# Kernel tuning notes

Measured on AMD Instinct MI355X. Metric: run time of the kernel, lower is better.

The kernel has to match this reference:

```python
import jax, jax.numpy as jnp
import numpy as np
import math

N = 2048          # rows (forced: input_dim_B // 2)
DB = 4096         # input_dim_B
DA = 5120         # input_dim_A
DX2 = DA - DB     # 1024, X2 feature dim
M1, M2 = 8, 4
DK, DV1, DV2 = 64, 64, 64
M = 512           # d_model of trailing encoder layers (nhead=1 inside)
LN_EPS = 1e-5


def setup_inputs() -> dict:
    key = jax.random.key(0)
    ks = jax.random.split(key, 24)
    s = 0.02
    f32 = jnp.float32
    inp = {
        "X1": jax.random.normal(ks[0], (N, DB), f32),
        "X2": jax.random.normal(ks[1], (N, DX2), f32),
        "X3": jax.random.normal(ks[2], (N, DB), f32),
        # Type-A heads (stacked over m1)
        "WQ": jax.random.normal(ks[3], (M1, DA, DK), f32) * s,
        "WK": jax.random.normal(ks[4], (M1, DA, DK), f32) * s,
        "WV": jax.random.normal(ks[5], (M1, DA, DV1), f32) * s,
        # Type-B heads (stacked over m2)
        "WVB": jax.random.normal(ks[6], (M2, DX2, DV2), f32) * s,
        "W_ali": jax.random.normal(ks[7], (DB, DB // 2), f32) * s,
        "W_O": jax.random.normal(ks[8], (M1 * DV1 + M2 * DV2, M), f32) * s,
        # two TransformerEncoderLayers (post-LN, nhead=1, relu FFN), stacked over layer dim
        "enc_Wq": jax.random.normal(ks[9], (2, M, M), f32) * s,
        "enc_Wk": jax.random.normal(ks[10], (2, M, M), f32) * s,
        "enc_Wv": jax.random.normal(ks[11], (2, M, M), f32) * s,
        "enc_bq": jnp.zeros((2, M), f32),
        "enc_bk": jnp.zeros((2, M), f32),
        "enc_bv": jnp.zeros((2, M), f32),
        "enc_Wo": jax.random.normal(ks[12], (2, M, M), f32) * s,
        "enc_bo": jnp.zeros((2, M), f32),
        "enc_ln1_g": jnp.ones((2, M), f32),
        "enc_ln1_b": jnp.zeros((2, M), f32),
        "enc_W1": jax.random.normal(ks[13], (2, M, DV1), f32) * s,
        "enc_b1": jnp.zeros((2, DV1), f32),
        "enc_W2": jax.random.normal(ks[14], (2, DV1, M), f32) * s,
        "enc_b2": jnp.zeros((2, M), f32),
        "enc_ln2_g": jnp.ones((2, M), f32),
        "enc_ln2_b": jnp.zeros((2, M), f32),
    }
    return inp


def _layer_norm(x, g, b):
    mu = jnp.mean(x, axis=-1, keepdims=True)
    var = jnp.mean(jnp.square(x - mu), axis=-1, keepdims=True)
    return (x - mu) * jax.lax.rsqrt(var + LN_EPS) * g + b


def _encoder_layer(x, Wq, bq, Wk, bk, Wv, bv, Wo, bo, g1, b1, W1, bW1, W2, bW2, g2, b2):
    # post-norm TransformerEncoderLayer, nhead=1, dropout in eval mode (off)
    q = x @ Wq + bq
    k = x @ Wk + bk
    v = x @ Wv + bv
    att = jax.nn.softmax((q @ k.T) / math.sqrt(M), axis=-1) @ v
    x = _layer_norm(x + (att @ Wo + bo), g1, b1)
    f = jax.nn.relu(x @ W1 + bW1) @ W2 + bW2
    return _layer_norm(x + f, g2, b2)


def reference(X1, X2, X3, WQ, WK, WV, WVB, W_ali, W_O,
              enc_Wq, enc_bq, enc_Wk, enc_bk, enc_Wv, enc_bv, enc_Wo, enc_bo,
              enc_ln1_g, enc_ln1_b, enc_W1, enc_b1, enc_W2, enc_b2, enc_ln2_g, enc_ln2_b):
    XA = jnp.concatenate([X1, X2], axis=1)  # [N, DA]
    # Type-A heads, batched over m1
    Q = jnp.einsum('nd,hdk->hnk', XA, WQ)
    K = jnp.einsum('nd,hdk->hnk', XA, WK)
    V = jnp.einsum('nd,hdv->hnv', XA, WV)
    scores = jnp.einsum('hnk,hmk->hnm', Q, K) / math.sqrt(DK)
    S = jax.nn.softmax(scores, axis=1)  # torch softmax(dim=0): over query/row axis
    ZA = jnp.einsum('hnm,hmv->hnv', S, V)             # [m1, N, dv1]
    ZA = jnp.transpose(ZA, (1, 0, 2)).reshape(N, M1 * DV1)
    # Type-B heads
    ali = jax.nn.sigmoid(X3) @ W_ali                  # [N, N] (DB//2 == N)
    zb = jnp.einsum('nd,hdv->hnv', X2, WVB)           # [m2, N, dv2]
    ZB = jnp.einsum('nm,hmv->hnv', ali, zb)
    ZB = jnp.transpose(ZB, (1, 0, 2)).reshape(N, M2 * DV2)
    Z = jnp.concatenate([ZA, ZB], axis=1) @ W_O       # [N, M]
    for l in range(2):
        Z = _encoder_layer(Z, enc_Wq[l], enc_bq[l], enc_Wk[l], enc_bk[l],
                           enc_Wv[l], enc_bv[l], enc_Wo[l], enc_bo[l],
                           enc_ln1_g[l], enc_ln1_b[l], enc_W1[l], enc_b1[l],
                           enc_W2[l], enc_b2[l], enc_ln2_g[l], enc_ln2_b[l])
    return Z
```

## Files before the change

kernel.cpp:

```cpp
#include <hip/hip_runtime.h>

#define DEV __device__ __forceinline__

typedef __attribute__((ext_vector_type(4))) float f32x4;
typedef __attribute__((ext_vector_type(8))) short s16x8;

DEV ushort f2b(float f) {
  union { float f; unsigned u; } x; x.f = f;
  unsigned r = (x.u + 0x7FFFu + ((x.u >> 16) & 1u)) >> 16;
  return (ushort)r;
}
DEV float b2f(ushort u) {
  union { unsigned u; float f; } x; x.u = ((unsigned)u) << 16;
  return x.f;
}

DEV void gload16(const ushort* g, ushort* l) {
  __builtin_amdgcn_global_load_lds(
      (const __attribute__((address_space(1))) unsigned int*)g,
      (__attribute__((address_space(3))) unsigned int*)l, 16, 0, 0);
}

struct PtrList { const float* p[4]; };

template<int BM, int BN, int BIAS, int ACT, bool OF, bool OB, int SKX,
         bool CSTAT, bool RSTAT, int NBUF>
__global__ __launch_bounds__(256) void gemm(
    const ushort* __restrict__ A, int lda, long long sA,
    const ushort* __restrict__ B, int ldb, long long sB,
    float* __restrict__ Cf, ushort* __restrict__ Cb, int ldc, long long sC,
    const float* __restrict__ bias, const float* __restrict__ bias2,
    float* __restrict__ pmo, float* __restrict__ pso,
    float scale0, float scale1, int K)
{
  constexpr int WM = BM / 2, WN = BN / 2, FM = WM / 16, FN = WN / 16;
  __shared__ __align__(16) ushort As[NBUF][BM * 64];
  __shared__ __align__(16) ushort Bs[NBUF][BN * 64];
  const int tid = threadIdx.x, l = tid & 63, w = tid >> 6;
  const int wr = w >> 1, wc = w & 1;
  const int gx = gridDim.x, gy = gridDim.y;
  const int nwg = gx * gy;
  const int orig = blockIdx.y * gx + blockIdx.x;
  const int xcd = orig & 7, rest = orig >> 3;
  const int q8 = nwg >> 3, r8 = nwg & 7;
  const int f = (xcd < r8 ? xcd * (q8 + 1) : r8 * (q8 + 1) + (xcd - r8) * q8) + rest;
  int bxr = f / gy;
  const int byy = f - bxr * gy;
  int ks = 0;
  if constexpr (SKX > 1) {
    const int nbx = gx / SKX;
    ks = bxr / nbx; bxr -= ks * nbx;
  }
  const int brow = byy * BM, bcol = bxr * BN;
  const long long z = blockIdx.z;
  A += z * sA + (size_t)ks * K;
  B += z * sB + (size_t)ks * K;
  const int lr = l & 15;
  const int sw = lr & 7, kh = l >> 4;
  f32x4 acc[FM][FN] = {};
  const int nk = K >> 6;

  auto stage = [&](int kt, int buf) {
    const int kof = kt << 6;
#pragma unroll
    for (int i = 0; i < BM / 32; ++i) {
      const int c = i * 256 + tid;
      const int r = c >> 3, k8 = c & 7;
      gload16(A + (size_t)(brow + r) * lda + kof + ((k8 ^ (r & 7)) << 3),
              &As[buf][i * 2048 + w * 512]);
    }
#pragma unroll
    for (int i = 0; i < BN / 32; ++i) {
      const int c = i * 256 + tid;
      const int r = c >> 3, k8 = c & 7;
      gload16(B + (size_t)(bcol + r) * ldb + kof + ((k8 ^ (r & 7)) << 3),
              &Bs[buf][i * 2048 + w * 512]);
    }
  };

  auto compute = [&](int kt, int buf) {
#pragma unroll
    for (int kk = 0; kk < 2; ++kk) {
      const int koff = ((kk * 4 + kh) ^ sw) << 3;
      s16x8 af[FM], bf[FN];
#pragma unroll
      for (int m = 0; m < FM; ++m)
        af[m] = *(const s16x8*)&As[buf][(wr * WM + m * 16 + lr) * 64 + koff];
#pragma unroll
      for (int n = 0; n < FN; ++n)
        bf[n] = *(const s16x8*)&Bs[buf][(wc * WN + n * 16 + lr) * 64 + koff];
#pragma unroll
      for (int m = 0; m < FM; ++m)
#pragma unroll
        for (int n = 0; n < FN; ++n)
          acc[m][n] = __builtin_amdgcn_mfma_f32_16x16x32_bf16(af[m], bf[n], acc[m][n], 0, 0, 0);
    }
  };

  if constexpr (NBUF == 2) {
    stage(0, 0);
    __syncthreads();
    for (int kt = 0; kt < nk - 1; ++kt) {
      stage(kt + 1, (kt + 1) & 1);
      compute(kt, kt & 1);
      __syncthreads();
    }
    compute(nk - 1, (nk - 1) & 1);
  } else {
    for (int kt = 0; kt < nk; ++kt) {
      stage(kt, 0);
      __syncthreads();
      compute(kt, 0);
      __syncthreads();
    }
  }

  if constexpr (OF || OB) {
    const float sc = (z == 0) ? scale0 : scale1;
    const float* bp = (z == 0) ? bias : bias2;
    const int cr = (l >> 4) * 4, cc = l & 15;
#pragma unroll
    for (int m = 0; m < FM; ++m) {
      const int r0 = brow + wr * WM + m * 16 + cr;
#pragma unroll
      for (int n = 0; n < FN; ++n) {
        const int gc = bcol + wc * WN + n * 16 + cc;
        float bc = 0.f;
        if constexpr (BIAS == 1) bc = bp[gc];
#pragma unroll
        for (int j = 0; j < 4; ++j) {
          float v = acc[m][n][j];
          if constexpr (BIAS == 1) v += bc;
          if constexpr (BIAS == 2) v += bp[r0 + j];
          v *= sc;
          if constexpr (ACT == 1) v = fmaxf(v, 0.f);
          const size_t off = (size_t)(r0 + j) * ldc + gc + (size_t)((z * SKX + ks) * sC);
          if constexpr (OF) Cf[off] = v;
          if constexpr (OB) Cb[off] = f2b(v);
        }
      }
    }
  }

  if constexpr (CSTAT) {
    __shared__ float sM[2][2][FN][16], sS[2][2][FN][16];
    float mx[FN], se[FN];
#pragma unroll
    for (int n = 0; n < FN; ++n) {
      float m0 = -3e38f;
#pragma unroll
      for (int m = 0; m < FM; ++m)
#pragma unroll
        for (int j = 0; j < 4; ++j) m0 = fmaxf(m0, acc[m][n][j]);
      float s0 = 0.f;
#pragma unroll
      for (int m = 0; m < FM; ++m)
#pragma unroll
        for (int j = 0; j < 4; ++j) s0 += __expf(acc[m][n][j] - m0);
      mx[n] = m0; se[n] = s0;
    }
#pragma unroll
    for (int o = 16; o <= 32; o <<= 1) {
#pragma unroll
      for (int n = 0; n < FN; ++n) {
        float m2 = __shfl_xor(mx[n], o), s2 = __shfl_xor(se[n], o);
        float M = fmaxf(mx[n], m2);
        se[n] = se[n] * __expf(mx[n] - M) + s2 * __expf(m2 - M);
        mx[n] = M;
      }
    }
    __syncthreads();
    if (l < 16) {
#pragma unroll
      for (int n = 0; n < FN; ++n) { sM[wr][wc][n][l] = mx[n]; sS[wr][wc][n][l] = se[n]; }
    }
    __syncthreads();
    if (wr == 0 && l < 16) {
#pragma unroll
      for (int n = 0; n < FN; ++n) {
        float m1 = sM[0][wc][n][l], m2 = sM[1][wc][n][l];
        float s1 = sS[0][wc][n][l], s2 = sS[1][wc][n][l];
        float M = fmaxf(m1, m2);
        float S = s1 * __expf(m1 - M) + s2 * __expf(m2 - M);
        const int gc = bcol + wc * 32 + n * 16 + l;
        const size_t o = ((size_t)(z * gy + byy)) * 2048 + gc;
        pmo[o] = M; pso[o] = S;
      }
    }
  }

  if constexpr (RSTAT) {
    __shared__ float sRM[2][2][WM], sRS[2][2][WM];
#pragma unroll
    for (int m = 0; m < FM; ++m) {
#pragma unroll
      for (int j = 0; j < 4; ++j) {
        float m0 = -3e38f;
#pragma unroll
        for (int n = 0; n < FN; ++n) m0 = fmaxf(m0, acc[m][n][j]);
        float s0 = 0.f;
#pragma unroll
        for (int n = 0; n < FN; ++n) s0 += __expf(acc[m][n][j] - m0);
#pragma unroll
        for (int o = 1; o <= 8; o <<= 1) {
          float m2 = __shfl_xor(m0, o), s2 = __shfl_xor(s0, o);
          float M = fmaxf(m0, m2);
          s0 = s0 * __expf(m0 - M) + s2 * __expf(m2 - M);
          m0 = M;
        }
        if ((l & 15) == 0) {
          sRM[wr][wc][m * 16 + (l >> 4) * 4 + j] = m0;
          sRS[wr][wc][m * 16 + (l >> 4) * 4 + j] = s0;
        }
      }
    }
    __syncthreads();
    if (wc == 0) {
      float m1 = sRM[wr][0][l], m2 = sRM[wr][1][l];
      float s1 = sRS[wr][0][l], s2 = sRS[wr][1][l];
      float M = fmaxf(m1, m2);
      float S = s1 * __expf(m1 - M) + s2 * __expf(m2 - M);
      const size_t o = (size_t)bxr * 2048 + brow + wr * WM + l;
      pmo[o] = M; pso[o] = S;
    }
  }
}

template<int MH, int NH>
DEV void qmfma2(const s16x8 (&Ax)[8], const s16x8 (&Bf)[4], f32x4 (&acc)[8][4]) {
#pragma unroll
  for (int kk = 0; kk < 2; ++kk)
#pragma unroll
    for (int m = 0; m < 4; ++m)
#pragma unroll
      for (int n = 0; n < 2; ++n)
        acc[MH * 4 + m][NH * 2 + n] = __builtin_amdgcn_mfma_f32_16x16x32_bf16(
            Ax[kk * 4 + m], Bf[kk * 2 + n], acc[MH * 4 + m][NH * 2 + n], 0, 0, 0);
}

DEV void tailwait(int c) {
  if (c == 1) { asm volatile("s_waitcnt vmcnt(4)" ::: "memory"); }
  else if (c == 2) { asm volatile("s_waitcnt vmcnt(0)" ::: "memory"); }
}

#define GBAR() asm volatile("s_barrier" ::: "memory")

template<int NBX>
__global__ __launch_bounds__(512, 2) void gemm256(
    const ushort* __restrict__ A, int lda,
    const ushort* __restrict__ B, int ldb,
    ushort* __restrict__ Cb, int ldc, long long sC, int Kc)
{
  __shared__ __align__(16) ushort As[2][2][8192];
  __shared__ __align__(16) ushort Bs[2][2][8192];
  const int tid = threadIdx.x, l = tid & 63, w = tid >> 6;
  const int wr = w >> 2, wc = w & 3;
  const int gx = gridDim.x, gy = gridDim.y;
  const int nwg = gx * gy;
  const int orig = blockIdx.y * gx + blockIdx.x;
  const int xcd = orig & 7, rest = orig >> 3;
  const int q8 = nwg >> 3, r8 = nwg & 7;
  const int f = (xcd < r8 ? xcd * (q8 + 1) : r8 * (q8 + 1) + (xcd - r8) * q8) + rest;
  int bxr = f / gy;
  const int byy = f - bxr * gy;
  const int ks = bxr / NBX; bxr -= ks * NBX;
  const int brow = byy * 256, bcol = bxr * 256;
  A += (size_t)ks * Kc;
  B += (size_t)ks * Kc;
  const int nk = Kc >> 6;
  const int lr = l & 15, kh = l >> 4, sw = lr & 7;
  const int arow = wr * 64 + lr, brw = wc * 32 + lr;

  const int r0 = tid >> 3, k80 = tid & 7;
  const size_t aoff = (size_t)(brow + r0) * lda + ((k80 ^ (r0 & 7)) << 3);
  const size_t boff = (size_t)(bcol + r0) * ldb + ((k80 ^ (r0 & 7)) << 3);

  f32x4 acc[8][4] = {};
  s16x8 Ax[8];
  s16x8 B0s[4], B1s[4];

  auto stA = [&](int kt, int buf, int half) {
    if (kt >= nk) return;
    const ushort* s = A + aoff + (size_t)(half * 128) * lda + (kt << 6);
    gload16(s, &As[buf][half][w * 512]);
    gload16(s + (size_t)64 * lda, &As[buf][half][4096 + w * 512]);
  };
  auto stB = [&](int kt, int buf, int half) {
    if (kt >= nk) return;
    const ushort* s = B + boff + (size_t)(half * 128) * ldb + (kt << 6);
    gload16(s, &Bs[buf][half][w * 512]);
    gload16(s + (size_t)64 * ldb, &Bs[buf][half][4096 + w * 512]);
  };
  auto rdA = [&](int buf, int half) {
#pragma unroll
    for (int kk = 0; kk < 2; ++kk) {
      const int koff = ((kk * 4 + kh) ^ sw) << 3;
#pragma unroll
      for (int m = 0; m < 4; ++m)
        Ax[kk * 4 + m] = *(const s16x8*)&As[buf][half][(arow + m * 16) * 64 + koff];
    }
  };
  auto rdB = [&](s16x8 (&dst)[4], int buf, int half) {
#pragma unroll
    for (int kk = 0; kk < 2; ++kk) {
      const int koff = ((kk * 4 + kh) ^ sw) << 3;
#pragma unroll
      for (int n = 0; n < 2; ++n)
        dst[kk * 2 + n] = *(const s16x8*)&Bs[buf][half][(brw + n * 16) * 64 + koff];
    }
  };

  stA(0, 0, 0); stB(0, 0, 0); stA(0, 0, 1); stB(0, 0, 1);
  stA(1, 1, 0); stB(1, 1, 0);
  asm volatile("s_waitcnt vmcnt(4)" ::: "memory");
  GBAR();
  rdA(0, 0); rdB(B0s, 0, 0);

  const int NT2 = nk >> 1;
#pragma unroll 1
  for (int j = 0; j < NT2; ++j) {
    const int tb = 2 * j + 1, ta2 = 2 * j + 2, tb2 = 2 * j + 3;
    const bool more = (ta2 < nk);
    stA(tb, 1, 1); GBAR();
    rdB(B1s, 0, 1);
    __builtin_amdgcn_s_setprio(1); qmfma2<0, 0>(Ax, B0s, acc); __builtin_amdgcn_s_setprio(0);
    GBAR();
    stB(tb, 1, 1); GBAR();
    __builtin_amdgcn_s_setprio(1); qmfma2<0, 1>(Ax, B1s, acc); __builtin_amdgcn_s_setprio(0);
    GBAR();
    stA(ta2, 0, 0); GBAR();
    rdA(0, 1);
    __builtin_amdgcn_s_setprio(1); qmfma2<1, 0>(Ax, B0s, acc); __builtin_amdgcn_s_setprio(0);
    GBAR();
    stB(ta2, 0, 0); GBAR();
    __builtin_amdgcn_s_setprio(1); qmfma2<1, 1>(Ax, B1s, acc); __builtin_amdgcn_s_setprio(0);
    tailwait(more ? 1 : 2); GBAR();
    rdA(1, 0); rdB(B0s, 1, 0);
    stA(ta2, 0, 1); GBAR();
    rdB(B1s, 1, 1);
    __builtin_amdgcn_s_setprio(1); qmfma2<0, 0>(Ax, B0s, acc); __builtin_amdgcn_s_setprio(0);
    GBAR();
    stB(ta2, 0, 1); GBAR();
    __builtin_amdgcn_s_setprio(1); qmfma2<0, 1>(Ax, B1s, acc); __builtin_amdgcn_s_setprio(0);
    GBAR();
    stA(tb2, 1, 0); GBAR();
    rdA(1, 1);
    __builtin_amdgcn_s_setprio(1); qmfma2<1, 0>(Ax, B0s, acc); __builtin_amdgcn_s_setprio(0);
    GBAR();
    stB(tb2, 1, 0); GBAR();
    __builtin_amdgcn_s_setprio(1); qmfma2<1, 1>(Ax, B1s, acc); __builtin_amdgcn_s_setprio(0);
    tailwait(more ? 1 : 0); GBAR();
    if (more) { rdA(0, 0); rdB(B0s, 0, 0); }
  }

  ushort* out = Cb + (size_t)ks * sC;
  const int cr = kh * 4, cc = lr;
#pragma unroll
  for (int mh = 0; mh < 2; ++mh)
#pragma unroll
    for (int m = 0; m < 4; ++m) {
      const int ro = brow + mh * 128 + wr * 64 + m * 16 + cr;
#pragma unroll
      for (int nh = 0; nh < 2; ++nh)
#pragma unroll
        for (int n = 0; n < 2; ++n) {
          const int gc = bcol + nh * 128 + wc * 32 + n * 16 + cc;
#pragma unroll
          for (int j2 = 0; j2 < 4; ++j2)
            out[(size_t)(ro + j2) * ldc + gc] = f2b(acc[mh * 4 + m][nh * 2 + n][j2]);
        }
    }
}

__global__ __launch_bounds__(256) void ffn_fused(
    const ushort* __restrict__ X, const ushort* __restrict__ W1,
    const float* __restrict__ b1, const ushort* __restrict__ W2T,
    const float* __restrict__ b2, float* __restrict__ Y)
{
  __shared__ __align__(16) ushort As[64 * 64];
  __shared__ __align__(16) ushort Bs[64 * 64];
  __shared__ __align__(16) ushort Hs[64 * 64];
  const int tid = threadIdx.x, l = tid & 63, w = tid >> 6;
  const int wr = w >> 1, wc = w & 1;
  const int bx = blockIdx.x, brow = blockIdx.y * 64;
  const int lr = l & 15, g = l >> 4, sw = lr & 7;
  f32x4 acc[2][2] = {};
  for (int kt = 0; kt < 8; ++kt) {
    const int kof = kt << 6;
#pragma unroll
    for (int i = 0; i < 2; ++i) {
      const int c = i * 256 + tid, r = c >> 3, k8 = c & 7;
      gload16(X + (size_t)(brow + r) * 512 + kof + ((k8 ^ (r & 7)) << 3),
              &As[i * 2048 + w * 512]);
    }
#pragma unroll
    for (int i = 0; i < 2; ++i) {
      const int c = i * 256 + tid, r = c >> 3, k8 = c & 7;
      gload16(W1 + (size_t)r * 512 + kof + ((k8 ^ (r & 7)) << 3),
              &Bs[i * 2048 + w * 512]);
    }
    __syncthreads();
#pragma unroll
    for (int kk = 0; kk < 2; ++kk) {
      const int koff = ((kk * 4 + g) ^ sw) << 3;
      s16x8 af[2], bf[2];
#pragma unroll
      for (int m = 0; m < 2; ++m) af[m] = *(const s16x8*)&As[(wr * 32 + m * 16 + lr) * 64 + koff];
#pragma unroll
      for (int n = 0; n < 2; ++n) bf[n] = *(const s16x8*)&Bs[(wc * 32 + n * 16 + lr) * 64 + koff];
#pragma unroll
      for (int m = 0; m < 2; ++m)
#pragma unroll
        for (int n = 0; n < 2; ++n)
          acc[m][n] = __builtin_amdgcn_mfma_f32_16x16x32_bf16(af[m], bf[n], acc[m][n], 0, 0, 0);
    }
    __syncthreads();
  }
#pragma unroll
  for (int m = 0; m < 2; ++m)
#pragma unroll
    for (int n = 0; n < 2; ++n) {
      const int col = wc * 32 + n * 16 + lr;
      const float bb = b1[col];
#pragma unroll
      for (int j = 0; j < 4; ++j) {
        const int row = wr * 32 + m * 16 + g * 4 + j;
        Hs[row * 64 + (((col >> 3) ^ (row & 7)) << 3) + (col & 7)] =
            f2b(fmaxf(acc[m][n][j] + bb, 0.f));
      }
    }
#pragma unroll
  for (int i = 0; i < 2; ++i) {
    const int c = i * 256 + tid, r = c >> 3, k8 = c & 7;
    gload16(W2T + (size_t)(bx * 64 + r) * 64 + ((k8 ^ (r & 7)) << 3),
            &Bs[i * 2048 + w * 512]);
  }
  __syncthreads();
  f32x4 acc2[2][2] = {};
#pragma unroll
  for (int kk = 0; kk < 2; ++kk) {
    const int koff = ((kk * 4 + g) ^ sw) << 3;
    s16x8 af[2], bf[2];
#pragma unroll
    for (int m = 0; m < 2; ++m) af[m] = *(const s16x8*)&Hs[(wr * 32 + m * 16 + lr) * 64 + koff];
#pragma unroll
    for (int n = 0; n < 2; ++n) bf[n] = *(const s16x8*)&Bs[(wc * 32 + n * 16 + lr) * 64 + koff];
#pragma unroll
    for (int m = 0; m < 2; ++m)
#pragma unroll
      for (int n = 0; n < 2; ++n)
        acc2[m][n] = __builtin_amdgcn_mfma_f32_16x16x32_bf16(af[m], bf[n], acc2[m][n], 0, 0, 0);
  }
#pragma unroll
  for (int m = 0; m < 2; ++m)
#pragma unroll
    for (int n = 0; n < 2; ++n) {
      const int gc = bx * 64 + wc * 32 + n * 16 + lr;
      const float bb = b2[gc];
#pragma unroll
      for (int j = 0; j < 4; ++j) {
        const int row = brow + wr * 32 + m * 16 + g * 4 + j;
        Y[(size_t)row * 512 + gc] = acc2[m][n][j] + bb;
      }
    }
}

__global__ __launch_bounds__(256) void pv_fused(
    const ushort* __restrict__ Q, const ushort* __restrict__ K,
    const ushort* __restrict__ Vt, const float* __restrict__ lse,
    ushort* __restrict__ ZAP)
{
  __shared__ __align__(16) ushort Qs[64 * 64];
  __shared__ __align__(16) ushort Ks[2][64 * 64];
  __shared__ __align__(16) ushort Vs[2][64 * 64];
  __shared__ __align__(16) ushort Ps[64 * 64];
  __shared__ float Ls[512];
  const int tid = threadIdx.x, l = tid & 63, w = tid >> 6;
  const int wr = w >> 1, wc = w & 1;
  const int h = blockIdx.z, brow = blockIdx.x * 64, ms = blockIdx.y;
  const int lr = l & 15, g = l >> 4, sw = lr & 7;

  auto stageKV = [&](int mc, int buf) {
#pragma unroll
    for (int i = 0; i < 2; ++i) {
      const int c = i * 256 + tid, r = c >> 3, k8 = c & 7;
      gload16(K + (size_t)(mc * 64 + r) * 512 + h * 64 + ((k8 ^ (r & 7)) << 3),
              &Ks[buf][i * 2048 + w * 512]);
    }
#pragma unroll
    for (int i = 0; i < 2; ++i) {
      const int c = i * 256 + tid, r = c >> 3, k8 = c & 7;
      gload16(Vt + (size_t)(h * 64 + r) * 2048 + mc * 64 + ((k8 ^ (r & 7)) << 3),
              &Vs[buf][i * 2048 + w * 512]);
    }
  };

#pragma unroll
  for (int i = 0; i < 2; ++i) {
    const int c = i * 256 + tid, r = c >> 3, k8 = c & 7;
    gload16(Q + (size_t)(brow + r) * 512 + h * 64 + ((k8 ^ (r & 7)) << 3),
            &Qs[i * 2048 + w * 512]);
  }
  stageKV(ms * 8, 0);
  for (int i = tid; i < 512; i += 256) Ls[i] = lse[h * 2048 + ms * 512 + i];
  __syncthreads();

  s16x8 aq[2][2];
#pragma unroll
  for (int nf = 0; nf < 2; ++nf)
#pragma unroll
    for (int kk = 0; kk < 2; ++kk)
      aq[nf][kk] = *(const s16x8*)&Qs[(wr * 32 + nf * 16 + lr) * 64 + (((kk * 4 + g) ^ sw) << 3)];

  f32x4 zacc[2][2] = {};
  for (int mi = 0; mi < 8; ++mi) {
    const int mc = ms * 8 + mi;
    const int buf = mi & 1;
    if (mi < 7) stageKV(mc + 1, buf ^ 1);
    f32x4 sacc[2][2] = {};
#pragma unroll
    for (int kk = 0; kk < 2; ++kk) {
      const int koff = ((kk * 4 + g) ^ sw) << 3;
      s16x8 bk[2];
#pragma unroll
      for (int mf = 0; mf < 2; ++mf)
        bk[mf] = *(const s16x8*)&Ks[buf][(wc * 32 + mf * 16 + lr) * 64 + koff];
#pragma unroll
      for (int nf = 0; nf < 2; ++nf)
#pragma unroll
        for (int mf = 0; mf < 2; ++mf)
          sacc[nf][mf] = __builtin_amdgcn_mfma_f32_16x16x32_bf16(aq[nf][kk], bk[mf], sacc[nf][mf], 0, 0, 0);
    }
#pragma unroll
    for (int nf = 0; nf < 2; ++nf)
#pragma unroll
      for (int mf = 0; mf < 2; ++mf) {
        const int m_loc = wc * 32 + mf * 16 + lr;
        const float lv = Ls[mi * 64 + m_loc];
#pragma unroll
        for (int j = 0; j < 4; ++j) {
          const int n_loc = wr * 32 + nf * 16 + g * 4 + j;
          Ps[n_loc * 64 + (((m_loc >> 3) ^ (n_loc & 7)) << 3) + (m_loc & 7)] =
              f2b(__expf(sacc[nf][mf][j] - lv));
        }
      }
    __syncthreads();
#pragma unroll
    for (int kk = 0; kk < 2; ++kk) {
      const int koff = ((kk * 4 + g) ^ sw) << 3;
      s16x8 pa[2], bv[2];
#pragma unroll
      for (int nf = 0; nf < 2; ++nf)
        pa[nf] = *(const s16x8*)&Ps[(wr * 32 + nf * 16 + lr) * 64 + koff];
#pragma unroll
      for (int vf = 0; vf < 2; ++vf)
        bv[vf] = *(const s16x8*)&Vs[buf][(wc * 32 + vf * 16 + lr) * 64 + koff];
#pragma unroll
      for (int nf = 0; nf < 2; ++nf)
#pragma unroll
        for (int vf = 0; vf < 2; ++vf)
          zacc[nf][vf] = __builtin_amdgcn_mfma_f32_16x16x32_bf16(pa[nf], bv[vf], zacc[nf][vf], 0, 0, 0);
    }
    __syncthreads();
  }
  ushort* out = ZAP + (size_t)ms * 2048 * 512;
#pragma unroll
  for (int nf = 0; nf < 2; ++nf)
#pragma unroll
    for (int vf = 0; vf < 2; ++vf)
#pragma unroll
      for (int j = 0; j < 4; ++j) {
        const int n = brow + wr * 32 + nf * 16 + g * 4 + j;
        const int col = h * 64 + wc * 32 + vf * 16 + lr;
        out[(size_t)n * 512 + col] = f2b(zacc[nf][vf][j]);
      }
}

template<int NS, int ACT>
__global__ __launch_bounds__(256) void reduceN(const ushort* __restrict__ P, long long sC,
    ushort* __restrict__ out, int cols, int ldout, long long zPoff, long long zOoff,
    int cshift, long long bstride, float scale, int scThresh, int rows,
    const float* __restrict__ bias)
{
  P += blockIdx.z * zPoff; out += blockIdx.z * zOoff;
  const int c4n = cols >> 2;
  const size_t total = (size_t)rows * c4n;
  for (size_t i = (size_t)blockIdx.x * 256 + threadIdx.x; i < total; i += (size_t)gridDim.x * 256) {
    const size_t r = i / c4n;
    const int c4 = (int)(i - r * c4n) << 2;
    float4 s = make_float4(0.f, 0.f, 0.f, 0.f);
#pragma unroll
    for (int k = 0; k < NS; ++k) {
      ushort4 t = *(const ushort4*)(P + (size_t)k * sC + r * cols + c4);
      s.x += b2f(t.x); s.y += b2f(t.y); s.z += b2f(t.z); s.w += b2f(t.w);
    }
    if constexpr (ACT == 1) {
      float4 bb = *(const float4*)(bias + c4);
      s.x = fmaxf(s.x + bb.x, 0.f); s.y = fmaxf(s.y + bb.y, 0.f);
      s.z = fmaxf(s.z + bb.z, 0.f); s.w = fmaxf(s.w + bb.w, 0.f);
    }
    const float sc = (c4 < scThresh) ? scale : 1.f;
    ushort4 o;
    o.x = f2b(s.x * sc); o.y = f2b(s.y * sc); o.z = f2b(s.z * sc); o.w = f2b(s.w * sc);
    const size_t oo = r * ldout + (size_t)(c4 >> cshift) * bstride + (c4 & ((1 << cshift) - 1));
    *(ushort4*)(out + oo) = o;
  }
}

__global__ __launch_bounds__(256) void prep_xab(const float* __restrict__ X1,
    const float* __restrict__ X2, ushort* __restrict__ XAb) {
  const size_t total = (size_t)2048 * 1280;
  for (size_t i = (size_t)blockIdx.x * 256 + threadIdx.x; i < total; i += (size_t)gridDim.x * 256) {
    const size_t r = i / 1280;
    const int c = (int)(i - r * 1280) << 2;
    float4 v = (c < 4096) ? *(const float4*)(X1 + r * 4096 + c)
                          : *(const float4*)(X2 + r * 1024 + (c - 4096));
    ushort4 o; o.x = f2b(v.x); o.y = f2b(v.y); o.z = f2b(v.z); o.w = f2b(v.w);
    *(ushort4*)(XAb + r * 5120 + c) = o;
  }
}

__global__ __launch_bounds__(256) void prep_x3w(const float* __restrict__ X3,
    const float* __restrict__ Wali, ushort* __restrict__ sX3,
    ushort* __restrict__ Walib) {
  const size_t n1 = (size_t)2048 * 1024;
  const size_t n2 = (size_t)4096 * 512;
  const size_t total = n1 + n2;
  for (size_t i = (size_t)blockIdx.x * 256 + threadIdx.x; i < total; i += (size_t)gridDim.x * 256) {
    if (i < n1) {
      const size_t r = i / 1024;
      const int c = (int)(i - r * 1024) << 2;
      float4 v = *(const float4*)(X3 + r * 4096 + c);
      v.x = 1.f / (1.f + __expf(-v.x)); v.y = 1.f / (1.f + __expf(-v.y));
      v.z = 1.f / (1.f + __expf(-v.z)); v.w = 1.f / (1.f + __expf(-v.w));
      ushort4 o; o.x = f2b(v.x); o.y = f2b(v.y); o.z = f2b(v.z); o.w = f2b(v.w);
      *(ushort4*)(sX3 + r * 4096 + c) = o;
    } else {
      const size_t j = i - n1;
      const size_t r = j / 512;
      const int c = (int)(j - r * 512) << 2;
      float4 v = *(const float4*)(Wali + r * 2048 + c);
      ushort4 o; o.x = f2b(v.x); o.y = f2b(v.y); o.z = f2b(v.z); o.w = f2b(v.w);
      *(ushort4*)(Walib + r * 2048 + c) = o;
    }
  }
}

__global__ __launch_bounds__(256) void expconv_row(const float* __restrict__ S,
    const float* __restrict__ pm, const float* __restrict__ ps, ushort* __restrict__ P) {
  const int r = blockIdx.x;
  float m = pm[(size_t)(threadIdx.x & 31) * 2048 + r];
  float s = ps[(size_t)(threadIdx.x & 31) * 2048 + r];
#pragma unroll
  for (int o = 1; o < 32; o <<= 1) {
    float m2 = __shfl_xor(m, o), s2 = __shfl_xor(s, o);
    float M = fmaxf(m, m2);
    s = s * __expf(m - M) + s2 * __expf(m2 - M);
    m = M;
  }
  const float L = m + __logf(s);
  const float* row = S + (size_t)r * 2048;
  ushort* pr = P + (size_t)r * 2048;
  for (int c = threadIdx.x * 4; c < 2048; c += 1024) {
    float4 v = *(const float4*)(row + c);
    ushort4 o4;
    o4.x = f2b(__expf(v.x - L)); o4.y = f2b(__expf(v.y - L));
    o4.z = f2b(__expf(v.z - L)); o4.w = f2b(__expf(v.w - L));
    *(ushort4*)(pr + c) = o4;
  }
}

__global__ __launch_bounds__(256) void colcombine(const float* __restrict__ pm,
    const float* __restrict__ ps, float* __restrict__ lse) {
  const int id = blockIdx.x * 256 + threadIdx.x;
  const int h = id >> 11, c = id & 2047;
  float M = -3e38f;
#pragma unroll
  for (int s = 0; s < 16; ++s) M = fmaxf(M, pm[((size_t)(h * 16 + s)) * 2048 + c]);
  float S = 0.f;
#pragma unroll
  for (int s = 0; s < 16; ++s) {
    size_t o = ((size_t)(h * 16 + s)) * 2048 + c;
    S += ps[o] * __expf(pm[o] - M);
  }
  lse[id] = M + __logf(S);
}

__global__ __launch_bounds__(256) void transpose_conv_multi(PtrList in, int zPerT,
    ushort* __restrict__ out, int R, int C) {
  __shared__ ushort t[32][33];
  const int z = blockIdx.z;
  const float* ip = in.p[z / zPerT] + (size_t)(z % zPerT) * R * C;
  ushort* op = out + (size_t)z * R * C;
  const int r0 = blockIdx.x * 32, c0 = blockIdx.y * 32;
#pragma unroll
  for (int i = 0; i < 4; ++i) {
    int r = r0 + threadIdx.y + i * 8;
    int c = c0 + threadIdx.x;
    float v = (r < R && c < C) ? ip[(size_t)r * C + c] : 0.f;
    t[threadIdx.x][threadIdx.y + i * 8] = f2b(v);
  }
  __syncthreads();
#pragma unroll
  for (int i = 0; i < 4; ++i) {
    int c = c0 + threadIdx.y + i * 8;
    int r = r0 + threadIdx.x;
    if (c < C && r < R) op[(size_t)c * R + r] = t[threadIdx.y + i * 8][threadIdx.x];
  }
}

__global__ __launch_bounds__(256) void transpose_conv_batch(
    const float* __restrict__ WVB, ushort* __restrict__ WVBT,
    const float* __restrict__ W_O, ushort* __restrict__ WOT,
    const float* __restrict__ eW1, ushort* __restrict__ EW1T,
    const float* __restrict__ eW2, ushort* __restrict__ EW2T) {
  __shared__ ushort t[32][33];
  const int b = blockIdx.x;
  const float* ip; ushort* op; int R, C, r0, c0;
  if (b < 256) {
    const int h = b >> 6, loc = b & 63;
    ip = WVB + (size_t)h * 65536; op = WVBT + (size_t)h * 65536;
    R = 1024; C = 64; r0 = (loc & 31) * 32; c0 = (loc >> 5) * 32;
  } else if (b < 640) {
    const int loc = b - 256;
    ip = W_O; op = WOT;
    R = 768; C = 512; r0 = (loc % 24) * 32; c0 = (loc / 24) * 32;
  } else if (b < 704) {
    const int loc = b - 640, lyr = loc >> 5, lo = loc & 31;
    ip = eW1 + (size_t)lyr * 32768; op = EW1T + (size_t)lyr * 32768;
    R = 512; C = 64; r0 = (lo & 15) * 32; c0 = (lo >> 4) * 32;
  } else {
    const int loc = b - 704, lyr = loc >> 5, lo = loc & 31;
    ip = eW2 + (size_t)lyr * 32768; op = EW2T + (size_t)lyr * 32768;
    R = 64; C = 512; r0 = (lo & 1) * 32; c0 = (lo >> 1) * 32;
  }
#pragma unroll
  for (int i = 0; i < 4; ++i) {
    int r = r0 + threadIdx.y + i * 8;
    int c = c0 + threadIdx.x;
    float v = (r < R && c < C) ? ip[(size_t)r * C + c] : 0.f;
    t[threadIdx.x][threadIdx.y + i * 8] = f2b(v);
  }
  __syncthreads();
#pragma unroll
  for (int i = 0; i < 4; ++i) {
    int c = c0 + threadIdx.y + i * 8;
    int r = r0 + threadIdx.x;
    if (c < C && r < R) op[(size_t)c * R + r] = t[threadIdx.y + i * 8][threadIdx.x];
  }
}

__global__ __launch_bounds__(256) void transpose_b16(const ushort* __restrict__ in,
    ushort* __restrict__ out, int R, int C) {
  __shared__ ushort t[32][33];
  const int r0 = blockIdx.x * 32, c0 = blockIdx.y * 32;
#pragma unroll
  for (int i = 0; i < 4; ++i)
    t[threadIdx.x][threadIdx.y + i * 8] = in[(size_t)(r0 + threadIdx.y + i * 8) * C + c0 + threadIdx.x];
  __syncthreads();
#pragma unroll
  for (int i = 0; i < 4; ++i)
    out[(size_t)(c0 + threadIdx.y + i * 8) * R + r0 + threadIdx.x] = t[threadIdx.y + i * 8][threadIdx.x];
}

__global__ __launch_bounds__(256) void ln_add(const float* __restrict__ X,
    const float* __restrict__ Y, const float* __restrict__ g, const float* __restrict__ b,
    float* __restrict__ of, ushort* __restrict__ ob) {
  const int r = blockIdx.x, t = threadIdx.x;
  const size_t base = (size_t)r * 512;
  float v0 = X[base + t] + Y[base + t];
  float v1 = X[base + t + 256] + Y[base + t + 256];
  float s = v0 + v1;
#pragma unroll
  for (int o = 1; o < 64; o <<= 1) s += __shfl_xor(s, o);
  __shared__ float sm[4], sq[4];
  const int l = t & 63, w = t >> 6;
  if (l == 0) sm[w] = s;
  __syncthreads();
  const float mu = (sm[0] + sm[1] + sm[2] + sm[3]) * (1.f / 512.f);
  const float d0 = v0 - mu, d1 = v1 - mu;
  float q = d0 * d0 + d1 * d1;
#pragma unroll
  for (int o = 1; o < 64; o <<= 1) q += __shfl_xor(q, o);
  if (l == 0) sq[w] = q;
  __syncthreads();
  const float var = (sq[0] + sq[1] + sq[2] + sq[3]) * (1.f / 512.f);
  const float rs = rsqrtf(var + 1e-5f);
  const float o0 = d0 * rs * g[t] + b[t];
  const float o1 = d1 * rs * g[t + 256] + b[t + 256];
  if (of) { of[base + t] = o0; of[base + t + 256] = o1; }
  if (ob) { ob[base + t] = f2b(o0); ob[base + t + 256] = f2b(o1); }
}

extern "C" void kernel_launch(void* const* d_in, const int* in_sizes, int n_in,
                              void* d_out, int out_size, void* d_ws, size_t ws_size,
                              hipStream_t stream) {
  (void)in_sizes; (void)n_in; (void)out_size;
  const float* X1   = (const float*)d_in[0];
  const float* X2   = (const float*)d_in[1];
  const float* X3   = (const float*)d_in[2];
  const float* WQ   = (const float*)d_in[3];
  const float* WK   = (const float*)d_in[4];
  const float* WV   = (const float*)d_in[5];
  const float* WVB  = (const float*)d_in[6];
  const float* Wali = (const float*)d_in[7];
  const float* W_O  = (const float*)d_in[8];
  const float* eWq  = (const float*)d_in[9];
  const float* eWk  = (const float*)d_in[10];
  const float* eWv  = (const float*)d_in[11];
  const float* ebq  = (const float*)d_in[12];
  const float* ebk  = (const float*)d_in[13];
  const float* ebv  = (const float*)d_in[14];
  const float* eWo  = (const float*)d_in[15];
  const float* ebo  = (const float*)d_in[16];
  const float* eg1  = (const float*)d_in[17];
  const float* ebl1 = (const float*)d_in[18];
  const float* eW1  = (const float*)d_in[19];
  const float* eB1  = (const float*)d_in[20];
  const float* eW2  = (const float*)d_in[21];
  const float* eB2  = (const float*)d_in[22];
  const float* eg2  = (const float*)d_in[23];
  const float* ebl2 = (const float*)d_in[24];
  float* OUT = (float*)d_out;
  char* ws = (char*)d_ws;

  const size_t oQB   = 0;
  const size_t oKB   = 2097152;
  const size_t oVB   = 4194304;
  const size_t oVTB  = 6291456;
  const size_t oZAB  = 8388608;
  const size_t oWOT  = 11534336;
  const size_t oEWQT = 12320768;
  const size_t oEWVT = 14417920;
  const size_t oEWOT = 15466496;
  const size_t oEW1T = 16515072;
  const size_t oEW2T = 16646144;
  const size_t oWVBT = 16777216;
  const size_t oZBT  = 17301504;
  const size_t oZ    = 18350080;
  const size_t oZB16 = 22544384;
  const size_t oX2F  = 24641536;
  const size_t oX2B  = 28835840;
  const size_t oY    = 30932992;
  const size_t oATT  = 35127296;
  const size_t oPM   = 37486592;
  const size_t oPS   = 38535168;
  const size_t oLSE  = 39583744;
  const size_t oDYN  = 39649280;
  const size_t oWQT  = oDYN;
  const size_t oQKVP = oDYN + 15728640;
  const size_t oZBP  = oDYN;
  const size_t oSX3  = oDYN;
  const size_t oWAB  = oDYN + 16777216;
  const size_t oW2P  = oDYN + 33554432;
  const size_t oW2T  = oDYN + 50331648;
  const size_t oZAP  = oDYN;
  const size_t oSCFe = oDYN;
  const size_t oPbe  = oDYN + 16777216;
  const size_t oATTP = oDYN + 50331648;
  if (ws_size < oDYN + 67108864) return;

  ushort* XAb  = (ushort*)(ws + oZ);
  ushort* WQT  = (ushort*)(ws + oWQT);
  ushort* QKVP = (ushort*)(ws + oQKVP);
  ushort* ZBP  = (ushort*)(ws + oZBP);
  ushort* sX3  = (ushort*)(ws + oSX3);
  ushort* Walib= (ushort*)(ws + oWAB);
  ushort* W2P  = (ushort*)(ws + oW2P);
  ushort* W2Tb = (ushort*)(ws + oW2T);
  ushort* ZBP2 = (ushort*)(ws + oW2P);
  ushort* ZAP  = (ushort*)(ws + oZAP);
  float*  SCFe = (float*)(ws + oSCFe);
  ushort* Pbe  = (ushort*)(ws + oPbe);
  ushort* ATTP = (ushort*)(ws + oATTP);
  ushort* Qb   = (ushort*)(ws + oQB);
  ushort* Kb   = (ushort*)(ws + oKB);
  ushort* Vb   = (ushort*)(ws + oVB);
  ushort* Vtb  = (ushort*)(ws + oVTB);
  ushort* ZABb = (ushort*)(ws + oZAB);
  ushort* WOT  = (ushort*)(ws + oWOT);
  ushort* EWQT = (ushort*)(ws + oEWQT);
  ushort* EWVT = (ushort*)(ws + oEWVT);
  ushort* EWOT = (ushort*)(ws + oEWOT);
  ushort* EW1T = (ushort*)(ws + oEW1T);
  ushort* EW2T = (ushort*)(ws + oEW2T);
  ushort* WVBT = (ushort*)(ws + oWVBT);
  ushort* ZBT  = (ushort*)(ws + oZBT);
  float*  Zf   = (float*)(ws + oZ);
  ushort* Zb16 = (ushort*)(ws + oZB16);
  float*  X2f  = (float*)(ws + oX2F);
  ushort* X2b  = (ushort*)(ws + oX2B);
  float*  Yf   = (float*)(ws + oY);
  ushort* ATTb = (ushort*)(ws + oATT);
  float*  PM   = (float*)(ws + oPM);
  float*  PS   = (float*)(ws + oPS);
  float*  LSE  = (float*)(ws + oLSE);

  const dim3 tb(32, 8);
  const float rs512 = 0.044194173824159216f;

  prep_xab<<<2048, 256, 0, stream>>>(X1, X2, XAb);
  {
    PtrList wqkv; wqkv.p[0] = WQ; wqkv.p[1] = WK; wqkv.p[2] = WV; wqkv.p[3] = nullptr;
    transpose_conv_multi<<<dim3(160, 2, 24), tb, 0, stream>>>(wqkv, 8, WQT, 5120, 64);
    PtrList enc4; enc4.p[0] = eWq; enc4.p[1] = eWk; enc4.p[2] = eWv; enc4.p[3] = eWo;
    transpose_conv_multi<<<dim3(16, 16, 8), tb, 0, stream>>>(enc4, 2, EWQT, 512, 512);
  }
  transpose_conv_batch<<<768, tb, 0, stream>>>(WVB, WVBT, W_O, WOT, eW1, EW1T, eW2, EW2T);

  gemm256<6><<<dim3(30, 8, 1), 512, 0, stream>>>(
      XAb, 5120, WQT, 5120, QKVP, 1536, 3145728LL, 1024);
  reduceN<5,0><<<1024, 256, 0, stream>>>(QKVP, 3145728LL, Qb, 1536, 512, 0, 0,
      9, 1048576LL, 0.125f, 512, 2048, nullptr);
  transpose_b16<<<dim3(64, 16), tb, 0, stream>>>(Vb, Vtb, 2048, 512);
  gemm<64,64,0,0,false,true,4,false,false,1><<<dim3(128,4,1), 256, 0, stream>>>(
      WVBT, 1024, 0, XAb + 4096, 5120, 0, nullptr, ZBP, 2048, 524288LL,
      nullptr, nullptr, nullptr, nullptr, 1.f, 1.f, 256);
  reduceN<4,0><<<1024, 256, 0, stream>>>(ZBP, 524288LL, ZBT, 2048, 2048, 0, 0,
      30, 0, 1.f, 0, 256, nullptr);

  prep_x3w<<<2048, 256, 0, stream>>>(X3, Wali, sX3, Walib);
  gemm<128,128,0,0,false,true,4,false,false,2><<<dim3(128,2,1), 256, 0, stream>>>(
      ZBT, 2048, 0, Walib, 2048, 0, nullptr, W2P, 4096, 1048576LL,
      nullptr, nullptr, nullptr, nullptr, 1.f, 1.f, 512);
  reduceN<4,0><<<512, 256, 0, stream>>>(W2P, 1048576LL, W2Tb, 4096, 4096, 0, 0,
      30, 0, 1.f, 0, 256, nullptr);
  gemm<128,64,0,0,false,true,8,false,false,1><<<dim3(32,16,1), 256, 0, stream>>>(
      sX3, 4096, 0, W2Tb, 4096, 0, nullptr, ZBP2, 256, 524288LL,
      nullptr, nullptr, nullptr, nullptr, 1.f, 1.f, 512);
  reduceN<8,0><<<512, 256, 0, stream>>>(ZBP2, 524288LL, ZABb + 512, 256, 768, 0, 0,
      30, 0, 1.f, 0, 2048, nullptr);

  gemm<128,64,0,0,false,false,1,true,false,1><<<dim3(32,16,8), 256, 0, stream>>>(
      Qb, 512, 64, Kb, 512, 64, nullptr, nullptr, 2048, 0,
      nullptr, nullptr, PM, PS, 1.f, 1.f, 64);
  colcombine<<<64, 256, 0, stream>>>(PM, PS, LSE);
  pv_fused<<<dim3(32, 4, 8), 256, 0, stream>>>(Qb, Kb, Vtb, LSE, ZAP);
  reduceN<4,0><<<1024, 256, 0, stream>>>(ZAP, 1048576LL, ZABb, 512, 768, 0, 0,
      30, 0, 1.f, 0, 2048, nullptr);

  gemm<64,64,0,0,true,true,1,false,false,2><<<dim3(8,32,1), 256, 0, stream>>>(
      ZABb, 768, 0, WOT, 768, 0, Zf, Zb16, 512, 0,
      nullptr, nullptr, nullptr, nullptr, 1.f, 1.f, 768);

  for (int lyr = 0; lyr < 2; ++lyr) {
    const ushort* wq = EWQT + (size_t)lyr * 262144;
    const ushort* wv = EWVT + (size_t)lyr * 262144;
    const ushort* wo = EWOT + (size_t)lyr * 262144;
    const ushort* w1 = EW1T + (size_t)lyr * 32768;
    const ushort* w2 = EW2T + (size_t)lyr * 32768;
    gemm<128,64,1,0,false,true,1,false,false,2><<<dim3(8,16,2), 256, 0, stream>>>(
        Zb16, 512, 0, wq, 512, 524288LL, nullptr, Qb, 512, 1048576LL,
        ebq + lyr * 512, ebk + lyr * 512, nullptr, nullptr, rs512, 1.f, 512);
    gemm<64,64,2,0,false,true,1,false,false,2><<<dim3(32,8,1), 256, 0, stream>>>(
        wv, 512, 0, Zb16, 512, 0, nullptr, Vtb, 2048, 0,
        ebv + lyr * 512, nullptr, nullptr, nullptr, 1.f, 1.f, 512);
    gemm<128,64,0,0,true,false,1,false,true,1><<<dim3(32,16,1), 256, 0, stream>>>(
        Qb, 512, 0, Kb, 512, 0, SCFe, nullptr, 2048, 0,
        nullptr, nullptr, PM, PS, 1.f, 1.f, 512);
    expconv_row<<<2048, 256, 0, stream>>>(SCFe, PM, PS, Pbe);
    gemm<128,64,0,0,false,true,4,false,false,1><<<dim3(32,16,1), 256, 0, stream>>>(
        Pbe, 2048, 0, Vtb, 2048, 0, nullptr, ATTP, 512, 1048576LL,
        nullptr, nullptr, nullptr, nullptr, 1.f, 1.f, 512);
    reduceN<4,0><<<1024, 256, 0, stream>>>(ATTP, 1048576LL, ATTb, 512, 512, 0, 0,
        30, 0, 1.f, 0, 2048, nullptr);
    gemm<64,64,1,0,true,false,1,false,false,2><<<dim3(8,32,1), 256, 0, stream>>>(
        ATTb, 512, 0, wo, 512, 0, Yf, nullptr, 512, 0,
        ebo + lyr * 512, nullptr, nullptr, nullptr, 1.f, 1.f, 512);
    ln_add<<<2048, 256, 0, stream>>>(Zf, Yf, eg1 + lyr * 512, ebl1 + lyr * 512, X2f, X2b);
    ffn_fused<<<dim3(8, 32), 256, 0, stream>>>(
        X2b, w1, eB1 + lyr * 64, w2, eB2 + lyr * 512, Yf);
    ln_add<<<2048, 256, 0, stream>>>(X2f, Yf, eg2 + lyr * 512, ebl2 + lyr * 512,
                                     (lyr == 0) ? Zf : OUT, (lyr == 0) ? Zb16 : nullptr);
  }
}
```

Before: 352.0 us.

## Fuse softmax exp into attention PV GEMM and drop split-K reduce

In the encoder layers, the row-softmax exponentiation is moved into the P·V GEMM. The new kernel reads fp32 scores, applies exp(s - lse), converts to bf16 in registers and feeds MFMA directly. This removes the bf16 P materialization, the split-K partial buffer and the reduceN pass. A small rowcombine kernel now computes the per-row logsumexp beforehand. The trade-off is a grid of only 256 blocks with full-K loops, which means less parallelism than the previous 4-way split-K, plus uncached fp32 score loads that are not staged through LDS.

```diff
diff --git a/kernel.cpp b/kernel.cpp
--- a/kernel.cpp
+++ b/kernel.cpp
@@ -576,6 +576,102 @@
       }
 }
 
+__global__ __launch_bounds__(256) void attp_fused(
+    const float* __restrict__ S, const float* __restrict__ lse,
+    const ushort* __restrict__ Vt, ushort* __restrict__ out)
+{
+  __shared__ __align__(16) ushort Bs[2][64 * 64];
+  const int tid = threadIdx.x, l = tid & 63, w = tid >> 6;
+  const int wr = w >> 1, wc = w & 1;
+  const int gx = gridDim.x, gy = gridDim.y;
+  const int nwg = gx * gy;
+  const int orig = blockIdx.y * gx + blockIdx.x;
+  const int xcd = orig & 7, rest = orig >> 3;
+  const int q8 = nwg >> 3, r8 = nwg & 7;
+  const int f = (xcd < r8 ? xcd * (q8 + 1) : r8 * (q8 + 1) + (xcd - r8) * q8) + rest;
+  const int bxr = f / gy;
+  const int byy = f - bxr * gy;
+  const int brow = byy * 64, bcol = bxr * 64;
+  const int lr = l & 15, kh = l >> 4, sw = lr & 7;
+  f32x4 acc[2][2] = {};
+  const float Lm0 = lse[brow + wr * 32 + lr];
+  const float Lm1 = lse[brow + wr * 32 + 16 + lr];
+
+  auto stageB = [&](int kt, int buf) {
+    const int kof = kt << 6;
+#pragma unroll
+    for (int i = 0; i < 2; ++i) {
+      const int c = i * 256 + tid, r = c >> 3, k8 = c & 7;
+      gload16(Vt + (size_t)(bcol + r) * 2048 + kof + ((k8 ^ (r & 7)) << 3),
+              &Bs[buf][i * 2048 + w * 512]);
+    }
+  };
+
+  stageB(0, 0);
+#pragma unroll 1
+  for (int kt = 0; kt < 32; ++kt) {
+    const int buf = kt & 1;
+    s16x8 pa[2][2];
+#pragma unroll
+    for (int m = 0; m < 2; ++m) {
+      const float L = (m == 0) ? Lm0 : Lm1;
+      const size_t rb = (size_t)(brow + wr * 32 + m * 16 + lr) * 2048 + (kt << 6) + kh * 8;
+#pragma unroll
+      for (int kk = 0; kk < 2; ++kk) {
+        float4 v0 = *(const float4*)(S + rb + kk * 32);
+        float4 v1 = *(const float4*)(S + rb + kk * 32 + 4);
+        s16x8 t;
+        t[0] = (short)f2b(__expf(v0.x - L)); t[1] = (short)f2b(__expf(v0.y - L));
+        t[2] = (short)f2b(__expf(v0.z - L)); t[3] = (short)f2b(__expf(v0.w - L));
+        t[4] = (short)f2b(__expf(v1.x - L)); t[5] = (short)f2b(__expf(v1.y - L));
+        t[6] = (short)f2b(__expf(v1.z - L)); t[7] = (short)f2b(__expf(v1.w - L));
+        pa[m][kk] = t;
+      }
+    }
+    __syncthreads();
+#pragma unroll
+    for (int kk = 0; kk < 2; ++kk) {
+      const int koff = ((kk * 4 + kh) ^ sw) << 3;
+      s16x8 bf[2];
+#pragma unroll
+      for (int n = 0; n < 2; ++n)
+        bf[n] = *(const s16x8*)&Bs[buf][(wc * 32 + n * 16 + lr) * 64 + koff];
+#pragma unroll
+      for (int m = 0; m < 2; ++m)
+#pragma unroll
+        for (int n = 0; n < 2; ++n)
+          acc[m][n] = __builtin_amdgcn_mfma_f32_16x16x32_bf16(pa[m][kk], bf[n], acc[m][n], 0, 0, 0);
+    }
+    if (kt < 31) stageB(kt + 1, buf ^ 1);
+  }
+
+  const int cr = kh * 4, cc = lr;
+#pragma unroll
+  for (int m = 0; m < 2; ++m)
+#pragma unroll
+    for (int n = 0; n < 2; ++n) {
+      const int gc = bcol + wc * 32 + n * 16 + cc;
+#pragma unroll
+      for (int j = 0; j < 4; ++j)
+        out[(size_t)(brow + wr * 32 + m * 16 + cr + j) * 512 + gc] = f2b(acc[m][n][j]);
+    }
+}
+
+__global__ __launch_bounds__(256) void rowcombine(const float* __restrict__ pm,
+    const float* __restrict__ ps, float* __restrict__ lse) {
+  const int r = blockIdx.x * 256 + threadIdx.x;
+  float M = -3e38f;
+#pragma unroll
+  for (int s = 0; s < 32; ++s) M = fmaxf(M, pm[(size_t)s * 2048 + r]);
+  float S = 0.f;
+#pragma unroll
+  for (int s = 0; s < 32; ++s) {
+    const size_t o = (size_t)s * 2048 + r;
+    S += ps[o] * __expf(pm[o] - M);
+  }
+  lse[r] = M + __logf(S);
+}
+
 template<int NS, int ACT>
 __global__ __launch_bounds__(256) void reduceN(const ushort* __restrict__ P, long long sC,
     ushort* __restrict__ out, int cols, int ldout, long long zPoff, long long zOoff,
@@ -643,30 +739,6 @@
       ushort4 o; o.x = f2b(v.x); o.y = f2b(v.y); o.z = f2b(v.z); o.w = f2b(v.w);
       *(ushort4*)(Walib + r * 2048 + c) = o;
     }
-  }
-}
-
-__global__ __launch_bounds__(256) void expconv_row(const float* __restrict__ S,
-    const float* __restrict__ pm, const float* __restrict__ ps, ushort* __restrict__ P) {
-  const int r = blockIdx.x;
-  float m = pm[(size_t)(threadIdx.x & 31) * 2048 + r];
-  float s = ps[(size_t)(threadIdx.x & 31) * 2048 + r];
-#pragma unroll
-  for (int o = 1; o < 32; o <<= 1) {
-    float m2 = __shfl_xor(m, o), s2 = __shfl_xor(s, o);
-    float M = fmaxf(m, m2);
-    s = s * __expf(m - M) + s2 * __expf(m2 - M);
-    m = M;
-  }
-  const float L = m + __logf(s);
-  const float* row = S + (size_t)r * 2048;
-  ushort* pr = P + (size_t)r * 2048;
-  for (int c = threadIdx.x * 4; c < 2048; c += 1024) {
-    float4 v = *(const float4*)(row + c);
-    ushort4 o4;
-    o4.x = f2b(__expf(v.x - L)); o4.y = f2b(__expf(v.y - L));
-    o4.z = f2b(__expf(v.z - L)); o4.w = f2b(__expf(v.w - L));
-    *(ushort4*)(pr + c) = o4;
   }
 }
 
@@ -856,8 +928,6 @@
   const size_t oW2T  = oDYN + 50331648;
   const size_t oZAP  = oDYN;
   const size_t oSCFe = oDYN;
-  const size_t oPbe  = oDYN + 16777216;
-  const size_t oATTP = oDYN + 50331648;
   if (ws_size < oDYN + 67108864) return;
 
   ushort* XAb  = (ushort*)(ws + oZ);
@@ -871,8 +941,6 @@
   ushort* ZBP2 = (ushort*)(ws + oW2P);
   ushort* ZAP  = (ushort*)(ws + oZAP);
   float*  SCFe = (float*)(ws + oSCFe);
-  ushort* Pbe  = (ushort*)(ws + oPbe);
-  ushort* ATTP = (ushort*)(ws + oATTP);
   ushort* Qb   = (ushort*)(ws + oQB);
   ushort* Kb   = (ushort*)(ws + oKB);
   ushort* Vb   = (ushort*)(ws + oVB);
@@ -958,12 +1026,8 @@
     gemm<128,64,0,0,true,false,1,false,true,1><<<dim3(32,16,1), 256, 0, stream>>>(
         Qb, 512, 0, Kb, 512, 0, SCFe, nullptr, 2048, 0,
         nullptr, nullptr, PM, PS, 1.f, 1.f, 512);
-    expconv_row<<<2048, 256, 0, stream>>>(SCFe, PM, PS, Pbe);
-    gemm<128,64,0,0,false,true,4,false,false,1><<<dim3(32,16,1), 256, 0, stream>>>(
-        Pbe, 2048, 0, Vtb, 2048, 0, nullptr, ATTP, 512, 1048576LL,
-        nullptr, nullptr, nullptr, nullptr, 1.f, 1.f, 512);
-    reduceN<4,0><<<1024, 256, 0, stream>>>(ATTP, 1048576LL, ATTb, 512, 512, 0, 0,
-        30, 0, 1.f, 0, 2048, nullptr);
+    rowcombine<<<8, 256, 0, stream>>>(PM, PS, LSE);
+    attp_fused<<<dim3(8, 32), 256, 0, stream>>>(SCFe, LSE, Vtb, ATTb);
     gemm<64,64,1,0,true,false,1,false,false,2><<<dim3(8,32,1), 256, 0, stream>>>(
         ATTb, 512, 0, wo, 512, 0, Yf, nullptr, 512, 0,
         ebo + lyr * 512, nullptr, nullptr, nullptr, 1.f, 1.f, 512);
```

After: 434.9 us. +23.5%, slower.

## Merge GEMM main-loop MFMA phases into four larger clusters with fewer barriers

Applied to the files above, without the earlier changes.

The 256x256 bf16 GEMM main loop is restructured from eight small MFMA clusters per iteration into four. Each new cluster covers both B halves, and the A and B LDS stores for a stage are issued together. The goal is to cut the number of workgroup barriers and phase switches, giving the scheduler longer stretches of MFMA work. In exchange, more LDS fragments are live in registers at once, and global-load issue is interleaved less finely with compute. The existing vmcnt waits must still match the new load order.

```diff
diff --git a/kernel.cpp b/kernel.cpp
--- a/kernel.cpp
+++ b/kernel.cpp
@@ -226,16 +226,22 @@
   }
 }
 
-template<int MH, int NH>
-DEV void qmfma2(const s16x8 (&Ax)[8], const s16x8 (&Bf)[4], f32x4 (&acc)[8][4]) {
+template<int MH>
+DEV void qmfma4(const s16x8 (&Ax)[8], const s16x8 (&B0s)[4], const s16x8 (&B1s)[4],
+                f32x4 (&acc)[8][4]) {
 #pragma unroll
   for (int kk = 0; kk < 2; ++kk)
 #pragma unroll
-    for (int m = 0; m < 4; ++m)
+    for (int m = 0; m < 4; ++m) {
 #pragma unroll
       for (int n = 0; n < 2; ++n)
-        acc[MH * 4 + m][NH * 2 + n] = __builtin_amdgcn_mfma_f32_16x16x32_bf16(
-            Ax[kk * 4 + m], Bf[kk * 2 + n], acc[MH * 4 + m][NH * 2 + n], 0, 0, 0);
+        acc[MH * 4 + m][n] = __builtin_amdgcn_mfma_f32_16x16x32_bf16(
+            Ax[kk * 4 + m], B0s[kk * 2 + n], acc[MH * 4 + m][n], 0, 0, 0);
+#pragma unroll
+      for (int n = 0; n < 2; ++n)
+        acc[MH * 4 + m][2 + n] = __builtin_amdgcn_mfma_f32_16x16x32_bf16(
+            Ax[kk * 4 + m], B1s[kk * 2 + n], acc[MH * 4 + m][2 + n], 0, 0, 0);
+    }
 }
 
 DEV void tailwait(int c) {
@@ -314,43 +320,34 @@
   stA(1, 1, 0); stB(1, 1, 0);
   asm volatile("s_waitcnt vmcnt(4)" ::: "memory");
   GBAR();
-  rdA(0, 0); rdB(B0s, 0, 0);
 
   const int NT2 = nk >> 1;
 #pragma unroll 1
   for (int j = 0; j < NT2; ++j) {
-    const int tb = 2 * j + 1, ta2 = 2 * j + 2, tb2 = 2 * j + 3;
-    const bool more = (ta2 < nk);
-    stA(tb, 1, 1); GBAR();
-    rdB(B1s, 0, 1);
-    __builtin_amdgcn_s_setprio(1); qmfma2<0, 0>(Ax, B0s, acc); __builtin_amdgcn_s_setprio(0);
+    const int t1 = 2 * j + 1, t2 = 2 * j + 2, t3 = 2 * j + 3;
+    const bool more = (t2 < nk);
+    rdA(0, 0); rdB(B0s, 0, 0); rdB(B1s, 0, 1);
+    stA(t1, 1, 1); stB(t1, 1, 1);
     GBAR();
-    stB(tb, 1, 1); GBAR();
-    __builtin_amdgcn_s_setprio(1); qmfma2<0, 1>(Ax, B1s, acc); __builtin_amdgcn_s_setprio(0);
+    __builtin_amdgcn_s_setprio(1); qmfma4<0>(Ax, B0s, B1s, acc); __builtin_amdgcn_s_setprio(0);
     GBAR();
-    stA(ta2, 0, 0); GBAR();
     rdA(0, 1);
-    __builtin_amdgcn_s_setprio(1); qmfma2<1, 0>(Ax, B0s, acc); __builtin_amdgcn_s_setprio(0);
+    stA(t2, 0, 0); stB(t2, 0, 0);
     GBAR();
-    stB(ta2, 0, 0); GBAR();
-    __builtin_amdgcn_s_setprio(1); qmfma2<1, 1>(Ax, B1s, acc); __builtin_amdgcn_s_setprio(0);
-    tailwait(more ? 1 : 2); GBAR();
-    rdA(1, 0); rdB(B0s, 1, 0);
-    stA(ta2, 0, 1); GBAR();
-    rdB(B1s, 1, 1);
-    __builtin_amdgcn_s_setprio(1); qmfma2<0, 0>(Ax, B0s, acc); __builtin_amdgcn_s_setprio(0);
+    __builtin_amdgcn_s_setprio(1); qmfma4<1>(Ax, B0s, B1s, acc); __builtin_amdgcn_s_setprio(0);
+    tailwait(more ? 1 : 2);
     GBAR();
-    stB(ta2, 0, 1); GBAR();
-    __builtin_amdgcn_s_setprio(1); qmfma2<0, 1>(Ax, B1s, acc); __builtin_amdgcn_s_setprio(0);
+    rdA(1, 0); rdB(B0s, 1, 0); rdB(B1s, 1, 1);
+    stA(t2, 0, 1); stB(t2, 0, 1);
     GBAR();
-    stA(tb2, 1, 0); GBAR();
+    __builtin_amdgcn_s_setprio(1); qmfma4<0>(Ax, B0s, B1s, acc); __builtin_amdgcn_s_setprio(0);
+    GBAR();
     rdA(1, 1);
-    __builtin_amdgcn_s_setprio(1); qmfma2<1, 0>(Ax, B0s, acc); __builtin_amdgcn_s_setprio(0);
+    stA(t3, 1, 0); stB(t3, 1, 0);
     GBAR();
-    stB(tb2, 1, 0); GBAR();
-    __builtin_amdgcn_s_setprio(1); qmfma2<1, 1>(Ax, B1s, acc); __builtin_amdgcn_s_setprio(0);
-    tailwait(more ? 1 : 0); GBAR();
-    if (more) { rdA(0, 0); rdB(B0s, 0, 0); }
+    __builtin_amdgcn_s_setprio(1); qmfma4<1>(Ax, B0s, B1s, acc); __builtin_amdgcn_s_setprio(0);
+    tailwait(more ? 1 : 0);
+    GBAR();
   }
 
   ushort* out = Cb + (size_t)ks * sC;
```

Measured after the change: 358.6 us. Within noise of the previous version (+1.9%).
